# Performance work log

Measured on AMD Instinct MI355X. Metric: run time of the kernel, lower is better.

The kernel has to match this reference:

```python
import jax, jax.numpy as jnp
import numpy as np

B, S, D = 8, 1024, 1024   # batch, routed-over rows, feature dim (input_dim)
E = 1024                  # output_dim (== S so gather indices are in range)
K = 2                     # top-k
ALPHA = 0.01


def setup_inputs() -> dict:
    key = jax.random.key(0)
    kx, kw = jax.random.split(key)
    x = jax.random.normal(kx, (B, S, D), dtype=jnp.float32)
    # nn.Linear(input_dim, output_dim, bias=False) weight: [E, D]
    W = jax.random.normal(kw, (E, D), dtype=jnp.float32) / np.sqrt(D).astype(np.float32)
    return {"x": x, "W": W}


def reference(x, W):
    # logits = proj(x): [B, S, E]  (temperature == 1.0 -> no scaling)
    logits = jnp.einsum('bsd,ed->bse', x, W)
    probs = jax.nn.softmax(logits, axis=-1)
    topk_probs, topk_idx = jax.lax.top_k(probs, K)            # [B, S, K]
    # router_selections: gather rows of x along dim 1 -> [B, S, K, D]
    sel = x[jnp.arange(B)[:, None, None], topk_idx]
    # y = sum_k topk_probs * selected rows -> [B, S, D]
    y = jnp.einsum('bsk,bskd->bsd', topk_probs, sel)
    # auxiliary load-balance loss
    router_probs = probs.mean(axis=(0, 1))                    # [E]
    counts = jnp.bincount(topk_idx.reshape(-1), length=E).astype(probs.dtype)
    router_fraction = counts / counts.sum()
    aux_loss = ALPHA * E * jnp.sum(router_probs * router_fraction)
    return y, aux_loss
```

## Files before the change

### kernel.cpp

```cpp
#include <hip/hip_runtime.h>

#define MTOK 8192
#define ED   1024

typedef short s16x8 __attribute__((ext_vector_type(8)));
typedef float f32x4 __attribute__((ext_vector_type(4)));
typedef int   i32x4 __attribute__((ext_vector_type(4)));
typedef unsigned short u16x4 __attribute__((ext_vector_type(4)));

__device__ __forceinline__ int cvtpk(float a, float b) {
    int r;
    asm("v_cvt_pk_bf16_f32 %0, %1, %2" : "=v"(r) : "v"(a), "v"(b));
    return r;
}

__device__ __forceinline__ void cvt_write(void* dstHi, void* dstLo,
                                          const float4 f0, const float4 f1) {
    i32x4 h, l;
    h[0] = cvtpk(f0.x, f0.y); h[1] = cvtpk(f0.z, f0.w);
    h[2] = cvtpk(f1.x, f1.y); h[3] = cvtpk(f1.z, f1.w);
    l[0] = cvtpk(f0.x - __builtin_bit_cast(float, h[0] << 16),
                 f0.y - __builtin_bit_cast(float, h[0] & 0xffff0000));
    l[1] = cvtpk(f0.z - __builtin_bit_cast(float, h[1] << 16),
                 f0.w - __builtin_bit_cast(float, h[1] & 0xffff0000));
    l[2] = cvtpk(f1.x - __builtin_bit_cast(float, h[2] << 16),
                 f1.y - __builtin_bit_cast(float, h[2] & 0xffff0000));
    l[3] = cvtpk(f1.z - __builtin_bit_cast(float, h[3] << 16),
                 f1.w - __builtin_bit_cast(float, h[3] & 0xffff0000));
    *(i32x4*)dstHi = h;
    *(i32x4*)dstLo = l;
}

__global__ __launch_bounds__(256) void wfrag_kernel(
        const float* __restrict__ W,
        unsigned short* __restrict__ Bhi, unsigned short* __restrict__ Blo) {
    const int task = blockIdx.x * 4 + (threadIdx.x >> 6);
    const int lane = threadIdx.x & 63;
    const int rowblk = task >> 5;
    const int kstep  = task & 31;
    const float* src = W + (size_t)(rowblk * 16 + (lane & 15)) * ED
                         + kstep * 32 + (lane >> 4) * 8;
    const float4 f0 = *(const float4*)src;
    const float4 f1 = *(const float4*)(src + 4);
    const size_t o = ((size_t)task * 64 + lane) * 8;
    cvt_write(&Bhi[o], &Blo[o], f0, f1);
}

__global__ __launch_bounds__(256, 2) void gemm_mfma_split_kernel(
        const float* __restrict__ Xf,
        const unsigned short* __restrict__ Bhi, const unsigned short* __restrict__ Blo,
        float* __restrict__ C) {
    __shared__ __align__(16) unsigned char smem[2 * 16384];

    const int bid = blockIdx.x;
    const int xcd = bid & 7;
    const int j   = bid >> 3;
    const int bm  = xcd * 8 + (j >> 3);
    const int bn  = j & 7;

    const int tid  = threadIdx.x;
    const int lane = tid & 63;
    const int wid  = tid >> 6;

    const int srow = lane >> 2;
    const int sg   = (lane & 3) ^ ((lane >> 3) & 3);
    const float* gA = Xf + (size_t)(bm * 128 + wid * 32 + srow) * ED + sg * 8;

    float4 fA0, fA1, fA2, fA3;
#define ALOAD(kk)                                                    \
    fA0 = *(const float4*)(gA + (kk));                               \
    fA1 = *(const float4*)(gA + (kk) + 4);                           \
    fA2 = *(const float4*)(gA + (kk) + 16 * 1024);                   \
    fA3 = *(const float4*)(gA + (kk) + 16 * 1024 + 4);

#define AWRITE(BOFF)                                                             \
    cvt_write(smem + (BOFF) + (2 * wid) * 1024 + lane * 16,                      \
              smem + (BOFF) + 8192 + (2 * wid) * 1024 + lane * 16, fA0, fA1);    \
    cvt_write(smem + (BOFF) + (2 * wid + 1) * 1024 + lane * 16,                  \
              smem + (BOFF) + 8192 + (2 * wid + 1) * 1024 + lane * 16, fA2, fA3);

    const int wm = wid >> 1, wn = wid & 1;
    const int fr = lane & 15, fg = lane >> 4;
    const int pg = fg ^ ((fr >> 1) & 3);
    const int aoff = (wm * 64 + fr) * 32 + pg * 8;

    const unsigned short* gBh = Bhi + (size_t)(bn * 8 + wn * 4) * 16384 + lane * 8;
    const unsigned short* gBl = Blo + (size_t)(bn * 8 + wn * 4) * 16384 + lane * 8;

    s16x8 bh0[4], bl0[4], bh1[4], bl1[4];
#define BLOAD(S, T)                                                  \
    _Pragma("unroll")                                                \
    for (int i = 0; i < 4; ++i) {                                    \
        bh##S[i] = *(const s16x8*)(gBh + i * 16384 + (T) * 512);     \
        bl##S[i] = *(const s16x8*)(gBl + i * 16384 + (T) * 512);     \
    }

    f32x4 acc[4][4] = {};

#define STEP(T, BUFOFF, S, SN)                                                   \
    {                                                                            \
        if ((T) < 31) { ALOAD(((T) + 1) * 32); BLOAD(SN, (T) + 1); }             \
        const unsigned short* Ah = (const unsigned short*)(smem + (BUFOFF));     \
        const unsigned short* Al = Ah + 4096;                                    \
        s16x8 ah[4], al[4];                                                      \
        _Pragma("unroll")                                                        \
        for (int i = 0; i < 4; ++i) {                                            \
            ah[i] = *(const s16x8*)&Ah[aoff + i * 512];                          \
            al[i] = *(const s16x8*)&Al[aoff + i * 512];                          \
        }                                                                        \
        _Pragma("unroll")                                                        \
        for (int i = 0; i < 4; ++i)                                              \
            _Pragma("unroll")                                                    \
            for (int jj = 0; jj < 4; ++jj) {                                     \
                acc[i][jj] = __builtin_amdgcn_mfma_f32_16x16x32_bf16(ah[i], bh##S[jj], acc[i][jj], 0, 0, 0); \
                acc[i][jj] = __builtin_amdgcn_mfma_f32_16x16x32_bf16(ah[i], bl##S[jj], acc[i][jj], 0, 0, 0); \
                acc[i][jj] = __builtin_amdgcn_mfma_f32_16x16x32_bf16(al[i], bh##S[jj], acc[i][jj], 0, 0, 0); \
            }                                                                    \
        if ((T) < 31) AWRITE((BUFOFF) ^ 16384);                                  \
        asm volatile("s_waitcnt lgkmcnt(0)" ::: "memory");                       \
        __builtin_amdgcn_s_barrier();                                            \
    }

    ALOAD(0);
    BLOAD(0, 0);
    AWRITE(0);
    asm volatile("s_waitcnt lgkmcnt(0)" ::: "memory");
    __builtin_amdgcn_s_barrier();

    for (int t2 = 0; t2 < 32; t2 += 2) {
        STEP(t2,     0,     0, 1)
        STEP(t2 + 1, 16384, 1, 0)
    }
#undef STEP
#undef BLOAD
#undef AWRITE
#undef ALOAD

    const int crow = bm * 128 + wm * 64 + fg * 4;
    const int ccol = bn * 128 + wn * 64 + fr;
#pragma unroll
    for (int i = 0; i < 4; ++i)
#pragma unroll
        for (int jj = 0; jj < 4; ++jj)
#pragma unroll
            for (int r = 0; r < 4; ++r)
                C[(size_t)(crow + i * 16 + r) * ED + ccol + jj * 16] = acc[i][jj][r];
}

#define BM 128
#define BN 128
#define BK 32
#define LDA (BM + 4)
#define LDB (BN + 4)

__global__ __launch_bounds__(256) void gemm_logits_kernel(const float* __restrict__ X,
                                                          const float* __restrict__ W,
                                                          float* __restrict__ C) {
    __shared__ float As[BK][LDA];
    __shared__ float Bs[BK][LDB];
    const int bm  = blockIdx.y * BM;
    const int bn  = blockIdx.x * BN;
    const int tid = threadIdx.x;
    const int tx  = tid & 15;
    const int ty  = tid >> 4;
    const int lr  = tid >> 3;
    const int lc  = (tid & 7) << 2;

    float acc[8][8];
#pragma unroll
    for (int i = 0; i < 8; ++i)
#pragma unroll
        for (int j = 0; j < 8; ++j) acc[i][j] = 0.f;

    for (int k0 = 0; k0 < ED; k0 += BK) {
#pragma unroll
        for (int i = 0; i < 4; ++i) {
            const int r = lr + i * 32;
            float4 va = *(const float4*)&X[(size_t)(bm + r) * ED + k0 + lc];
            As[lc + 0][r] = va.x; As[lc + 1][r] = va.y;
            As[lc + 2][r] = va.z; As[lc + 3][r] = va.w;
            float4 vb = *(const float4*)&W[(size_t)(bn + r) * ED + k0 + lc];
            Bs[lc + 0][r] = vb.x; Bs[lc + 1][r] = vb.y;
            Bs[lc + 2][r] = vb.z; Bs[lc + 3][r] = vb.w;
        }
        __syncthreads();
#pragma unroll
        for (int kk = 0; kk < BK; ++kk) {
            float a[8], b[8];
            *(float4*)&a[0] = *(const float4*)&As[kk][ty * 8];
            *(float4*)&a[4] = *(const float4*)&As[kk][ty * 8 + 4];
            *(float4*)&b[0] = *(const float4*)&Bs[kk][tx * 8];
            *(float4*)&b[4] = *(const float4*)&Bs[kk][tx * 8 + 4];
#pragma unroll
            for (int i = 0; i < 8; ++i)
#pragma unroll
                for (int j = 0; j < 8; ++j)
                    acc[i][j] = fmaf(a[i], b[j], acc[i][j]);
        }
        __syncthreads();
    }
#pragma unroll
    for (int i = 0; i < 8; ++i) {
        const int r = bm + ty * 8 + i;
        float4* dst = (float4*)&C[(size_t)r * ED + bn + tx * 8];
        dst[0] = make_float4(acc[i][0], acc[i][1], acc[i][2], acc[i][3]);
        dst[1] = make_float4(acc[i][4], acc[i][5], acc[i][6], acc[i][7]);
    }
}

__device__ __forceinline__ bool better(float v, int i, float bv, int bi) {
    return (v > bv) || (v == bv && i < bi);
}

__global__ __launch_bounds__(256, 8) void softmax_wave_kernel(
        const float* __restrict__ X, float* __restrict__ OUT,
        float* __restrict__ partial, int* __restrict__ counts) {
    __shared__ float L[4 * 1024];
    const int tid  = threadIdx.x;
    const int lane = tid & 63;
    const int w    = tid >> 6;
    const int t    = blockIdx.x * 4 + w;

    const float4* row4 = (const float4*)&OUT[(size_t)t * ED];
    float4 p[4];
#pragma unroll
    for (int i = 0; i < 4; ++i) p[i] = row4[lane + 64 * i];

    float v1 = -1e30f, v2 = -1e30f; int i1 = 0x7fffffff, i2 = 0x7fffffff;
#pragma unroll
    for (int i = 0; i < 4; ++i) {
        const float vv[4] = {p[i].x, p[i].y, p[i].z, p[i].w};
#pragma unroll
        for (int c = 0; c < 4; ++c) {
            const int e = 256 * i + 4 * lane + c;
            const float v = vv[c];
            if (better(v, e, v1, i1)) { v2 = v1; i2 = i1; v1 = v; i1 = e; }
            else if (better(v, e, v2, i2)) { v2 = v; i2 = e; }
        }
    }
#pragma unroll
    for (int off = 32; off; off >>= 1) {
        const float ov1 = __shfl_xor(v1, off); const int oi1 = __shfl_xor(i1, off);
        const float ov2 = __shfl_xor(v2, off); const int oi2 = __shfl_xor(i2, off);
        if (better(ov1, oi1, v1, i1)) {
            float nv2; int ni2;
            if (better(v1, i1, ov2, oi2)) { nv2 = v1; ni2 = i1; }
            else { nv2 = ov2; ni2 = oi2; }
            v1 = ov1; i1 = oi1; v2 = nv2; i2 = ni2;
        } else if (better(ov1, oi1, v2, i2)) { v2 = ov1; i2 = oi1; }
    }
    const float m = v1;

    float s = 0.f;
#pragma unroll
    for (int i = 0; i < 4; ++i) {
        p[i].x = __expf(p[i].x - m); p[i].y = __expf(p[i].y - m);
        p[i].z = __expf(p[i].z - m); p[i].w = __expf(p[i].w - m);
        s += p[i].x + p[i].y + p[i].z + p[i].w;
    }
#pragma unroll
    for (int off = 32; off; off >>= 1) s += __shfl_xor(s, off);
    const float inv = 1.f / s;

#pragma unroll
    for (int i = 0; i < 4; ++i) {
        float4 q = make_float4(p[i].x * inv, p[i].y * inv, p[i].z * inv, p[i].w * inv);
        *(float4*)&L[w * 1024 + i * 256 + lane * 4] = q;
    }

    const float p1 = inv;
    const float p2 = __expf(v2 - m) * inv;
    const int b = t >> 10;
    const float4* x1 = (const float4*)&X[((size_t)(b << 10) + i1) * ED];
    const float4* x2 = (const float4*)&X[((size_t)(b << 10) + i2) * ED];
    float4* yrow = (float4*)&OUT[(size_t)t * ED];
#pragma unroll
    for (int i = 0; i < 4; ++i) {
        const int idx = lane + 64 * i;
        const float4 a = x1[idx];
        const float4 c = x2[idx];
        float4 r;
        r.x = fmaf(p1, a.x, p2 * c.x);
        r.y = fmaf(p1, a.y, p2 * c.y);
        r.z = fmaf(p1, a.z, p2 * c.z);
        r.w = fmaf(p1, a.w, p2 * c.w);
        yrow[idx] = r;
    }

    if (lane == 0) { atomicAdd(&counts[i1], 1); atomicAdd(&counts[i2], 1); }

    __syncthreads();
    float4 s0 = *(float4*)&L[0 * 1024 + tid * 4];
    float4 s1 = *(float4*)&L[1 * 1024 + tid * 4];
    float4 s2 = *(float4*)&L[2 * 1024 + tid * 4];
    float4 s3 = *(float4*)&L[3 * 1024 + tid * 4];
    float4 r;
    r.x = (s0.x + s1.x) + (s2.x + s3.x);
    r.y = (s0.y + s1.y) + (s2.y + s3.y);
    r.z = (s0.z + s1.z) + (s2.z + s3.z);
    r.w = (s0.w + s1.w) + (s2.w + s3.w);
    *(float4*)&partial[(size_t)blockIdx.x * 1024 + tid * 4] = r;
}

__global__ __launch_bounds__(256) void aux1_kernel(const float* __restrict__ partial,
                                                   const int* __restrict__ counts,
                                                   float* __restrict__ dotPartial) {
    __shared__ float red[16][16];
    const int tid = threadIdx.x;
    const int el  = tid & 15;
    const int ch  = tid >> 4;
    const int e   = blockIdx.x * 16 + el;
    float s = 0.f;
    for (int k = 0; k < 128; ++k)
        s += partial[(size_t)(ch * 128 + k) * 1024 + e];
    red[ch][el] = s;
    __syncthreads();
    if (tid < 16) {
        float rs = 0.f;
#pragma unroll
        for (int c = 0; c < 16; ++c) rs += red[c][tid];
        float val = rs * (float)counts[blockIdx.x * 16 + tid];
#pragma unroll
        for (int off = 8; off; off >>= 1) val += __shfl_xor(val, off);
        if (tid == 0) dotPartial[blockIdx.x] = val;
    }
}

__global__ void aux2_kernel(const float* __restrict__ dotPartial, float* __restrict__ out) {
    const int lane = threadIdx.x;
    float v = dotPartial[lane];
#pragma unroll
    for (int off = 32; off; off >>= 1) v += __shfl_xor(v, off);
    if (lane == 0)
        out[(size_t)MTOK * ED] = v * (0.01f * 1024.f / (8192.f * 16384.f));
}

#define TOKS_PER_BLK 16
__global__ __launch_bounds__(256) void softmax_topk_y_kernel(
        const float* __restrict__ X, float* __restrict__ OUT,
        float* __restrict__ router_sum, int* __restrict__ counts) {
    __shared__ float routerLocal[ED];
    __shared__ float redMax[4];
    __shared__ float redSum[4];
    __shared__ float wV1[4]; __shared__ int wI1[4];
    __shared__ float wV2[4]; __shared__ int wI2[4];

    const int tid  = threadIdx.x;
    const int lane = tid & 63;
    const int wave = tid >> 6;

    for (int e = tid; e < ED; e += 256) routerLocal[e] = 0.f;
    __syncthreads();

    const int t0 = blockIdx.x * TOKS_PER_BLK;
    for (int t = t0; t < t0 + TOKS_PER_BLK; ++t) {
        const float* lrow = &OUT[(size_t)t * ED];
        float l[4];
#pragma unroll
        for (int i = 0; i < 4; ++i) l[i] = lrow[tid + i * 256];

        float m = fmaxf(fmaxf(l[0], l[1]), fmaxf(l[2], l[3]));
#pragma unroll
        for (int off = 32; off; off >>= 1) m = fmaxf(m, __shfl_xor(m, off));
        if (lane == 0) redMax[wave] = m;
        __syncthreads();
        m = fmaxf(fmaxf(redMax[0], redMax[1]), fmaxf(redMax[2], redMax[3]));

        float p[4]; float s = 0.f;
#pragma unroll
        for (int i = 0; i < 4; ++i) { p[i] = expf(l[i] - m); s += p[i]; }
#pragma unroll
        for (int off = 32; off; off >>= 1) s += __shfl_xor(s, off);
        if (lane == 0) redSum[wave] = s;

        float v1 = -1e30f, v2 = -1e30f; int i1 = 0x7fffffff, i2 = 0x7fffffff;
#pragma unroll
        for (int i = 0; i < 4; ++i) {
            const float v = l[i]; const int ix = tid + i * 256;
            if (better(v, ix, v1, i1)) { v2 = v1; i2 = i1; v1 = v; i1 = ix; }
            else if (better(v, ix, v2, i2)) { v2 = v; i2 = ix; }
        }
#pragma unroll
        for (int off = 32; off; off >>= 1) {
            const float ov1 = __shfl_xor(v1, off); const int oi1 = __shfl_xor(i1, off);
            const float ov2 = __shfl_xor(v2, off); const int oi2 = __shfl_xor(i2, off);
            if (better(ov1, oi1, v1, i1)) {
                float nv2; int ni2;
                if (better(v1, i1, ov2, oi2)) { nv2 = v1; ni2 = i1; }
                else { nv2 = ov2; ni2 = oi2; }
                v1 = ov1; i1 = oi1; v2 = nv2; i2 = ni2;
            } else if (better(ov1, oi1, v2, i2)) { v2 = ov1; i2 = oi1; }
        }
        if (lane == 0) { wV1[wave] = v1; wI1[wave] = i1; wV2[wave] = v2; wI2[wave] = i2; }
        __syncthreads();

        v1 = wV1[0]; i1 = wI1[0]; v2 = wV2[0]; i2 = wI2[0];
#pragma unroll
        for (int w = 1; w < 4; ++w) {
            const float ov1 = wV1[w]; const int oi1 = wI1[w];
            const float ov2 = wV2[w]; const int oi2 = wI2[w];
            if (better(ov1, oi1, v1, i1)) {
                float nv2; int ni2;
                if (better(v1, i1, ov2, oi2)) { nv2 = v1; ni2 = i1; }
                else { nv2 = ov2; ni2 = oi2; }
                v1 = ov1; i1 = oi1; v2 = nv2; i2 = ni2;
            } else if (better(ov1, oi1, v2, i2)) { v2 = ov1; i2 = oi1; }
        }
        const float stot = redSum[0] + redSum[1] + redSum[2] + redSum[3];
        const float inv = 1.f / stot;

#pragma unroll
        for (int i = 0; i < 4; ++i) routerLocal[tid + i * 256] += p[i] * inv;

        const float p1 = expf(v1 - m) * inv;
        const float p2 = expf(v2 - m) * inv;

        const int b = t >> 10;
        const float4* x1 = (const float4*)&X[((size_t)(b << 10) + i1) * ED];
        const float4* x2 = (const float4*)&X[((size_t)(b << 10) + i2) * ED];
        float4* yrow = (float4*)&OUT[(size_t)t * ED];
        const float4 a = x1[tid];
        const float4 c = x2[tid];
        float4 r;
        r.x = fmaf(p1, a.x, p2 * c.x);
        r.y = fmaf(p1, a.y, p2 * c.y);
        r.z = fmaf(p1, a.z, p2 * c.z);
        r.w = fmaf(p1, a.w, p2 * c.w);
        yrow[tid] = r;

        if (tid == 0) { atomicAdd(&counts[i1], 1); atomicAdd(&counts[i2], 1); }
        __syncthreads();
    }

    for (int e = tid; e < ED; e += 256) atomicAdd(&router_sum[e], routerLocal[e]);
}

__global__ __launch_bounds__(256) void aux_kernel(const float* __restrict__ router_sum,
                                                  const int* __restrict__ counts,
                                                  float* __restrict__ out) {
    __shared__ float red[4];
    const int tid = threadIdx.x;
    float s = 0.f;
    for (int e = tid; e < ED; e += 256)
        s += (router_sum[e] * (1.f / 8192.f)) * ((float)counts[e] * (1.f / 16384.f));
#pragma unroll
    for (int off = 32; off; off >>= 1) s += __shfl_xor(s, off);
    if ((tid & 63) == 0) red[tid >> 6] = s;
    __syncthreads();
    if (tid == 0) out[(size_t)MTOK * ED] = 0.01f * 1024.f * (red[0] + red[1] + red[2] + red[3]);
}

extern "C" void kernel_launch(void* const* d_in, const int* in_sizes, int n_in,
                              void* d_out, int out_size, void* d_ws, size_t ws_size,
                              hipStream_t stream) {
    const float* X = (const float*)d_in[0];
    const float* W = (const float*)d_in[1];
    float* out = (float*)d_out;

    const size_t WS_NEED = (size_t)ED * ED * 2 * sizeof(unsigned short)
                         + (size_t)2048 * 1024 * sizeof(float)
                         + 64 * sizeof(float) + ED * sizeof(int);

    if (ws_size >= WS_NEED) {
        unsigned short* Bhi = (unsigned short*)d_ws;
        unsigned short* Blo = Bhi + (size_t)ED * ED;
        float* partial      = (float*)(Blo + (size_t)ED * ED);
        float* dotPartial   = partial + (size_t)2048 * 1024;
        int*   counts       = (int*)(dotPartial + 64);

        hipMemsetAsync(counts, 0, ED * sizeof(int), stream);
        wfrag_kernel<<<512, 256, 0, stream>>>(W, Bhi, Blo);
        gemm_mfma_split_kernel<<<512, 256, 0, stream>>>(X, Bhi, Blo, out);
        softmax_wave_kernel<<<MTOK / 4, 256, 0, stream>>>(X, out, partial, counts);
        aux1_kernel<<<64, 256, 0, stream>>>(partial, counts, dotPartial);
        aux2_kernel<<<1, 64, 0, stream>>>(dotPartial, out);
    } else {
        float* router_sum = (float*)d_ws;
        int*   counts     = (int*)((char*)d_ws + ED * sizeof(float));
        hipMemsetAsync(d_ws, 0, ED * (sizeof(float) + sizeof(int)), stream);
        dim3 ggrid(ED / BN, MTOK / BM);
        gemm_logits_kernel<<<ggrid, 256, 0, stream>>>(X, W, out);
        softmax_topk_y_kernel<<<MTOK / TOKS_PER_BLK, 256, 0, stream>>>(X, out, router_sum, counts);
        aux_kernel<<<1, 256, 0, stream>>>(router_sum, counts, out);
    }
}
```

Baseline: 93.72 us.

## Pre-convert X into bf16 hi/lo MFMA fragments and drop LDS staging in GEMM

```diff
diff --git a/kernel.cpp b/kernel.cpp
--- a/kernel.cpp
+++ b/kernel.cpp
@@ -31,111 +31,76 @@
     *(i32x4*)dstLo = l;
 }
 
-__global__ __launch_bounds__(256) void wfrag_kernel(
-        const float* __restrict__ W,
-        unsigned short* __restrict__ Bhi, unsigned short* __restrict__ Blo) {
+__global__ __launch_bounds__(256) void frag_kernel(
+        const float* __restrict__ M,
+        unsigned short* __restrict__ Fhi, unsigned short* __restrict__ Flo) {
     const int task = blockIdx.x * 4 + (threadIdx.x >> 6);
     const int lane = threadIdx.x & 63;
     const int rowblk = task >> 5;
     const int kstep  = task & 31;
-    const float* src = W + (size_t)(rowblk * 16 + (lane & 15)) * ED
+    const float* src = M + (size_t)(rowblk * 16 + (lane & 15)) * ED
                          + kstep * 32 + (lane >> 4) * 8;
     const float4 f0 = *(const float4*)src;
     const float4 f1 = *(const float4*)(src + 4);
     const size_t o = ((size_t)task * 64 + lane) * 8;
-    cvt_write(&Bhi[o], &Blo[o], f0, f1);
-}
-
-__global__ __launch_bounds__(256, 2) void gemm_mfma_split_kernel(
-        const float* __restrict__ Xf,
+    cvt_write(&Fhi[o], &Flo[o], f0, f1);
+}
+
+__global__ __launch_bounds__(256, 2) void gemm_frag_kernel(
+        const unsigned short* __restrict__ Ahi, const unsigned short* __restrict__ Alo,
         const unsigned short* __restrict__ Bhi, const unsigned short* __restrict__ Blo,
         float* __restrict__ C) {
-    __shared__ __align__(16) unsigned char smem[2 * 16384];
-
     const int bid = blockIdx.x;
     const int xcd = bid & 7;
     const int j   = bid >> 3;
     const int bm  = xcd * 8 + (j >> 3);
     const int bn  = j & 7;
 
-    const int tid  = threadIdx.x;
-    const int lane = tid & 63;
-    const int wid  = tid >> 6;
-
-    const int srow = lane >> 2;
-    const int sg   = (lane & 3) ^ ((lane >> 3) & 3);
-    const float* gA = Xf + (size_t)(bm * 128 + wid * 32 + srow) * ED + sg * 8;
-
-    float4 fA0, fA1, fA2, fA3;
-#define ALOAD(kk)                                                    \
-    fA0 = *(const float4*)(gA + (kk));                               \
-    fA1 = *(const float4*)(gA + (kk) + 4);                           \
-    fA2 = *(const float4*)(gA + (kk) + 16 * 1024);                   \
-    fA3 = *(const float4*)(gA + (kk) + 16 * 1024 + 4);
-
-#define AWRITE(BOFF)                                                             \
-    cvt_write(smem + (BOFF) + (2 * wid) * 1024 + lane * 16,                      \
-              smem + (BOFF) + 8192 + (2 * wid) * 1024 + lane * 16, fA0, fA1);    \
-    cvt_write(smem + (BOFF) + (2 * wid + 1) * 1024 + lane * 16,                  \
-              smem + (BOFF) + 8192 + (2 * wid + 1) * 1024 + lane * 16, fA2, fA3);
-
+    const int lane = threadIdx.x & 63;
+    const int wid  = threadIdx.x >> 6;
     const int wm = wid >> 1, wn = wid & 1;
+
+    const size_t laneo = (size_t)lane * 8;
+    const unsigned short* gAh = Ahi + (size_t)(bm * 8 + wm * 4) * 16384 + laneo;
+    const unsigned short* gAl = Alo + (size_t)(bm * 8 + wm * 4) * 16384 + laneo;
+    const unsigned short* gBh = Bhi + (size_t)(bn * 8 + wn * 4) * 16384 + laneo;
+    const unsigned short* gBl = Blo + (size_t)(bn * 8 + wn * 4) * 16384 + laneo;
+
+    s16x8 ah0[4], al0[4], bh0[4], bl0[4];
+    s16x8 ah1[4], al1[4], bh1[4], bl1[4];
+
+#define LOADSET(S, T)                                                  \
+    _Pragma("unroll")                                                  \
+    for (int i = 0; i < 4; ++i) {                                      \
+        ah##S[i] = *(const s16x8*)(gAh + i * 16384 + (T) * 512);       \
+        al##S[i] = *(const s16x8*)(gAl + i * 16384 + (T) * 512);       \
+        bh##S[i] = *(const s16x8*)(gBh + i * 16384 + (T) * 512);       \
+        bl##S[i] = *(const s16x8*)(gBl + i * 16384 + (T) * 512);       \
+    }
+
+#define MFMASET(S)                                                     \
+    _Pragma("unroll")                                                  \
+    for (int i = 0; i < 4; ++i)                                        \
+        _Pragma("unroll")                                              \
+        for (int jj = 0; jj < 4; ++jj) {                               \
+            acc[i][jj] = __builtin_amdgcn_mfma_f32_16x16x32_bf16(ah##S[i], bh##S[jj], acc[i][jj], 0, 0, 0); \
+            acc[i][jj] = __builtin_amdgcn_mfma_f32_16x16x32_bf16(ah##S[i], bl##S[jj], acc[i][jj], 0, 0, 0); \
+            acc[i][jj] = __builtin_amdgcn_mfma_f32_16x16x32_bf16(al##S[i], bh##S[jj], acc[i][jj], 0, 0, 0); \
+        }
+
+    f32x4 acc[4][4] = {};
+
+    LOADSET(0, 0);
+    for (int t2 = 0; t2 < 32; t2 += 2) {
+        LOADSET(1, t2 + 1);
+        MFMASET(0);
+        if (t2 + 2 < 32) LOADSET(0, t2 + 2);
+        MFMASET(1);
+    }
+#undef LOADSET
+#undef MFMASET
+
     const int fr = lane & 15, fg = lane >> 4;
-    const int pg = fg ^ ((fr >> 1) & 3);
-    const int aoff = (wm * 64 + fr) * 32 + pg * 8;
-
-    const unsigned short* gBh = Bhi + (size_t)(bn * 8 + wn * 4) * 16384 + lane * 8;
-    const unsigned short* gBl = Blo + (size_t)(bn * 8 + wn * 4) * 16384 + lane * 8;
-
-    s16x8 bh0[4], bl0[4], bh1[4], bl1[4];
-#define BLOAD(S, T)                                                  \
-    _Pragma("unroll")                                                \
-    for (int i = 0; i < 4; ++i) {                                    \
-        bh##S[i] = *(const s16x8*)(gBh + i * 16384 + (T) * 512);     \
-        bl##S[i] = *(const s16x8*)(gBl + i * 16384 + (T) * 512);     \
-    }
-
-    f32x4 acc[4][4] = {};
-
-#define STEP(T, BUFOFF, S, SN)                                                   \
-    {                                                                            \
-        if ((T) < 31) { ALOAD(((T) + 1) * 32); BLOAD(SN, (T) + 1); }             \
-        const unsigned short* Ah = (const unsigned short*)(smem + (BUFOFF));     \
-        const unsigned short* Al = Ah + 4096;                                    \
-        s16x8 ah[4], al[4];                                                      \
-        _Pragma("unroll")                                                        \
-        for (int i = 0; i < 4; ++i) {                                            \
-            ah[i] = *(const s16x8*)&Ah[aoff + i * 512];                          \
-            al[i] = *(const s16x8*)&Al[aoff + i * 512];                          \
-        }                                                                        \
-        _Pragma("unroll")                                                        \
-        for (int i = 0; i < 4; ++i)                                              \
-            _Pragma("unroll")                                                    \
-            for (int jj = 0; jj < 4; ++jj) {                                     \
-                acc[i][jj] = __builtin_amdgcn_mfma_f32_16x16x32_bf16(ah[i], bh##S[jj], acc[i][jj], 0, 0, 0); \
-                acc[i][jj] = __builtin_amdgcn_mfma_f32_16x16x32_bf16(ah[i], bl##S[jj], acc[i][jj], 0, 0, 0); \
-                acc[i][jj] = __builtin_amdgcn_mfma_f32_16x16x32_bf16(al[i], bh##S[jj], acc[i][jj], 0, 0, 0); \
-            }                                                                    \
-        if ((T) < 31) AWRITE((BUFOFF) ^ 16384);                                  \
-        asm volatile("s_waitcnt lgkmcnt(0)" ::: "memory");                       \
-        __builtin_amdgcn_s_barrier();                                            \
-    }
-
-    ALOAD(0);
-    BLOAD(0, 0);
-    AWRITE(0);
-    asm volatile("s_waitcnt lgkmcnt(0)" ::: "memory");
-    __builtin_amdgcn_s_barrier();
-
-    for (int t2 = 0; t2 < 32; t2 += 2) {
-        STEP(t2,     0,     0, 1)
-        STEP(t2 + 1, 16384, 1, 0)
-    }
-#undef STEP
-#undef BLOAD
-#undef AWRITE
-#undef ALOAD
-
     const int crow = bm * 128 + wm * 64 + fg * 4;
     const int ccol = bn * 128 + wn * 64 + fr;
 #pragma unroll
@@ -457,20 +422,23 @@
     const float* W = (const float*)d_in[1];
     float* out = (float*)d_out;
 
-    const size_t WS_NEED = (size_t)ED * ED * 2 * sizeof(unsigned short)
-                         + (size_t)2048 * 1024 * sizeof(float)
+    const size_t WS_NEED = (size_t)MTOK * ED * 2 * sizeof(unsigned short)
+                         + (size_t)ED * ED * 2 * sizeof(unsigned short)
                          + 64 * sizeof(float) + ED * sizeof(int);
 
     if (ws_size >= WS_NEED) {
-        unsigned short* Bhi = (unsigned short*)d_ws;
-        unsigned short* Blo = Bhi + (size_t)ED * ED;
-        float* partial      = (float*)(Blo + (size_t)ED * ED);
-        float* dotPartial   = partial + (size_t)2048 * 1024;
+        unsigned short* Xfh = (unsigned short*)d_ws;
+        unsigned short* Xfl = Xfh + (size_t)MTOK * ED;
+        unsigned short* Wfh = Xfl + (size_t)MTOK * ED;
+        unsigned short* Wfl = Wfh + (size_t)ED * ED;
+        float* dotPartial   = (float*)(Wfl + (size_t)ED * ED);
         int*   counts       = (int*)(dotPartial + 64);
+        float* partial      = (float*)Xfh;
 
         hipMemsetAsync(counts, 0, ED * sizeof(int), stream);
-        wfrag_kernel<<<512, 256, 0, stream>>>(W, Bhi, Blo);
-        gemm_mfma_split_kernel<<<512, 256, 0, stream>>>(X, Bhi, Blo, out);
+        frag_kernel<<<4096, 256, 0, stream>>>(X, Xfh, Xfl);
+        frag_kernel<<<512, 256, 0, stream>>>(W, Wfh, Wfl);
+        gemm_frag_kernel<<<512, 256, 0, stream>>>(Xfh, Xfl, Wfh, Wfl, out);
         softmax_wave_kernel<<<MTOK / 4, 256, 0, stream>>>(X, out, partial, counts);
         aux1_kernel<<<64, 256, 0, stream>>>(partial, counts, dotPartial);
         aux2_kernel<<<1, 64, 0, stream>>>(dotPartial, out);
```

New measurement: 108.6 us. 15.8% more time.
